# Performance work log

Hardware: AMD Instinct MI355X
Metric: run time of the kernel (lower is better)

Reference implementation:

```python
import jax, jax.numpy as jnp
import numpy as np

N = 100000
E = 3200000
NFEAT, NHID, NCLASS = 512, 64, 64
K = 10
ALPHA = 0.1


def setup_inputs() -> dict:
    key = jax.random.key(0)
    ks = jax.random.split(key, 8)
    x = jax.random.normal(ks[0], (N, NFEAT), dtype=jnp.float32)
    edge_index = jax.random.randint(ks[1], (2, E), 0, N, dtype=jnp.int32)
    s1 = 1.0 / np.sqrt(NFEAT)
    W1 = jax.random.uniform(ks[2], (NFEAT, NHID), jnp.float32, -s1, s1)
    b1 = jax.random.uniform(ks[3], (NHID,), jnp.float32, -s1, s1)
    s2 = 1.0 / np.sqrt(NHID)
    W2 = jax.random.uniform(ks[4], (NHID, NCLASS), jnp.float32, -s2, s2)
    b2 = jax.random.uniform(ks[5], (NCLASS,), jnp.float32, -s2, s2)
    # PPR init of gamma coefficients: temp[k] = alpha*(1-alpha)^k, temp[K] = (1-alpha)^K
    temp = ALPHA * (1.0 - ALPHA) ** np.arange(K + 1)
    temp[-1] = (1.0 - ALPHA) ** K
    temp = jnp.asarray(temp, dtype=jnp.float32)
    return {"x": x, "edge_index": edge_index, "W1": W1, "b1": b1, "W2": W2, "b2": b2, "temp": temp}


def _gcn_norm(edge_index, num_nodes):
    # add self loops, weight 1 (PyG gcn_norm defaults)
    loop = jnp.arange(num_nodes, dtype=edge_index.dtype)
    src = jnp.concatenate([edge_index[0], loop])
    dst = jnp.concatenate([edge_index[1], loop])
    w = jnp.ones(src.shape[0], dtype=jnp.float32)
    deg = jax.ops.segment_sum(w, dst, num_segments=num_nodes)
    dinv = jnp.where(deg > 0, jax.lax.rsqrt(deg), 0.0)
    norm = dinv[src] * w * dinv[dst]
    return src, dst, norm


def reference(x, edge_index, W1, b1, W2, b2, temp):
    # MLP part (eval mode, dropout is identity)
    h = jax.nn.relu(x @ W1 + b1) @ W2 + b2  # [N, nclass]
    src, dst, norm = _gcn_norm(edge_index, x.shape[0])
    hidden = h * temp[0]
    for k in range(K):
        # gather-scale-scatter: h <- A_hat @ h
        h = jax.ops.segment_sum(norm[:, None] * h[src], dst, num_segments=x.shape[0])
        hidden = hidden + temp[k + 1] * h
    return hidden
```

## Files before the change

### kernel.cpp

```cpp
#include <hip/hip_runtime.h>

static constexpr int N = 100000;
static constexpr int E = 3200000;
static constexpr int NFEAT = 512;
static constexpr int K = 10;

typedef _Float16 half8 __attribute__((ext_vector_type(8)));
typedef _Float16 half4v __attribute__((ext_vector_type(4)));
typedef float v2f __attribute__((ext_vector_type(2)));
typedef unsigned int uint2v __attribute__((ext_vector_type(2)));

static constexpr size_t OFF_CNT    = 0;
static constexpr size_t OFF_FILL   = 512ull * 1024;
static constexpr size_t OFF_ROWPTR = 1024ull * 1024;
static constexpr size_t OFF_DINV   = 1536ull * 1024;
static constexpr size_t OFF_BSUM   = 2048ull * 1024;
static constexpr size_t OFF_EW     = 2560ull * 1024;
static constexpr size_t OFF_G16    = OFF_EW + (size_t)E * 4 + 1024;
static constexpr size_t OFF_GA     = OFF_G16 + (size_t)N * 64 * 2 + 1024;
static constexpr size_t OFF_GB     = OFF_GA + (size_t)N * 64 + 1024;
static constexpr size_t OFF_SCA    = OFF_GB + (size_t)N * 64 + 1024;
static constexpr size_t OFF_SCB    = OFF_SCA + (size_t)N * 4 + 1024;
static constexpr size_t OFF_H1     = OFF_SCB + (size_t)N * 4 + 1024;

__global__ __launch_bounds__(256) void count_k(const int* __restrict__ dst,
                                               int* __restrict__ cnt) {
  int e = blockIdx.x * 256 + threadIdx.x;
  if (e < E) atomicAdd(&cnt[__builtin_nontemporal_load(dst + e)], 1);
}

__global__ __launch_bounds__(256) void dinv_k(const int* __restrict__ cnt,
                                              float* __restrict__ dinv) {
  int i = blockIdx.x * 256 + threadIdx.x;
  if (i < N) dinv[i] = 1.0f / sqrtf((float)(cnt[i] + 1));
}

__device__ inline int wave_incl_scan(int x) {
  int lane = threadIdx.x & 63;
#pragma unroll
  for (int off = 1; off < 64; off <<= 1) {
    int y = __shfl_up(x, off, 64);
    if (lane >= off) x += y;
  }
  return x;
}

__global__ __launch_bounds__(256) void scan1_k(const int* __restrict__ cnt,
                                               int* __restrict__ rowptr,
                                               int* __restrict__ bsum) {
  __shared__ int wsum[4];
  int tid = threadIdx.x, wid = tid >> 6, lane = tid & 63;
  int base = blockIdx.x * 1024 + tid * 4;
  int4 v = {0, 0, 0, 0};
  if (base + 3 < N) {
    v = *(const int4*)(cnt + base);
  } else {
    if (base + 0 < N) v.x = cnt[base + 0];
    if (base + 1 < N) v.y = cnt[base + 1];
    if (base + 2 < N) v.z = cnt[base + 2];
    if (base + 3 < N) v.w = cnt[base + 3];
  }
  int tsum = v.x + v.y + v.z + v.w;
  int incl = wave_incl_scan(tsum);
  if (lane == 63) wsum[wid] = incl;
  __syncthreads();
  int wof = 0;
  for (int i = 0; i < wid; ++i) wof += wsum[i];
  int e0 = wof + incl - tsum;
  if (base + 0 < N) rowptr[base + 0] = e0;
  if (base + 1 < N) rowptr[base + 1] = e0 + v.x;
  if (base + 2 < N) rowptr[base + 2] = e0 + v.x + v.y;
  if (base + 3 < N) rowptr[base + 3] = e0 + v.x + v.y + v.z;
  if (tid == 255) bsum[blockIdx.x] = wof + incl;
}

__global__ __launch_bounds__(128) void scan2_k(int* __restrict__ bsum) {
  __shared__ int w0sum;
  int tid = threadIdx.x, wid = tid >> 6, lane = tid & 63;
  int v = (tid < 98) ? bsum[tid] : 0;
  int incl = wave_incl_scan(v);
  if (wid == 0 && lane == 63) w0sum = incl;
  __syncthreads();
  int excl = incl - v + (wid ? w0sum : 0);
  if (tid < 98) bsum[tid] = excl;
}

__global__ __launch_bounds__(256) void scan3_k(int* __restrict__ rowptr,
                                               const int* __restrict__ bsum) {
  int i = blockIdx.x * 256 + threadIdx.x;
  if (i < N) rowptr[i] += bsum[blockIdx.x >> 2];
  if (i == 0) rowptr[N] = E;
}

__global__ __launch_bounds__(256) void fill2_k(const int* __restrict__ src,
                                               const int* __restrict__ dst,
                                               const int* __restrict__ rowptr,
                                               int* __restrict__ fillc,
                                               int* __restrict__ es) {
  const int slice = blockIdx.x & 7;
  const int chunk = blockIdx.x >> 3;
  const int lo = slice * 12500;
  const int hi = lo + 12500;
  int e = chunk * 4096 + threadIdx.x;
  const int eend = min(E, chunk * 4096 + 4096);
  for (; e < eend; e += 256) {
    int d = __builtin_nontemporal_load(dst + e);
    if (d >= lo && d < hi) {
      int pos = rowptr[d] + atomicAdd(&fillc[d], 1);
      es[pos] = __builtin_nontemporal_load(src + e);
    }
  }
}

__global__ __launch_bounds__(256) void gemm1_k(const float* __restrict__ x,
                                               const float* __restrict__ W1,
                                               const float* __restrict__ b1,
                                               _Float16* __restrict__ h1) {
  __shared__ float xs[16][256];
  __shared__ float w1s[16 * 64];
  const int tid = threadIdx.x;
  const int n0 = blockIdx.x * 256;
  const int tn = tid & 127;
  const int jh = tid >> 7;
  float4 acca[8], accb[8];
#pragma unroll
  for (int i = 0; i < 8; ++i) {
    acca[i] = float4{0.f, 0.f, 0.f, 0.f};
    accb[i] = float4{0.f, 0.f, 0.f, 0.f};
  }
  const int rowA = min(n0 + tid, N - 1);
  const float* xr = x + (size_t)rowA * NFEAT;
  for (int k0 = 0; k0 < NFEAT; k0 += 16) {
    float4 a0 = *(const float4*)(xr + k0 + 0);
    float4 a1 = *(const float4*)(xr + k0 + 4);
    float4 a2 = *(const float4*)(xr + k0 + 8);
    float4 a3 = *(const float4*)(xr + k0 + 12);
    float4 wv = *(const float4*)(W1 + (size_t)k0 * 64 + tid * 4);
    __syncthreads();
    xs[0][tid] = a0.x;  xs[1][tid] = a0.y;  xs[2][tid] = a0.z;  xs[3][tid] = a0.w;
    xs[4][tid] = a1.x;  xs[5][tid] = a1.y;  xs[6][tid] = a1.z;  xs[7][tid] = a1.w;
    xs[8][tid] = a2.x;  xs[9][tid] = a2.y;  xs[10][tid] = a2.z; xs[11][tid] = a2.w;
    xs[12][tid] = a3.x; xs[13][tid] = a3.y; xs[14][tid] = a3.z; xs[15][tid] = a3.w;
    *(float4*)&w1s[tid * 4] = wv;
    __syncthreads();
#pragma unroll
    for (int kk = 0; kk < 16; ++kk) {
      float xa = xs[kk][tn];
      float xb = xs[kk][tn + 128];
      const float* wr = &w1s[kk * 64 + jh * 32];
#pragma unroll
      for (int jj = 0; jj < 8; ++jj) {
        float4 w4 = *(const float4*)(wr + jj * 4);
        acca[jj].x += xa * w4.x; acca[jj].y += xa * w4.y;
        acca[jj].z += xa * w4.z; acca[jj].w += xa * w4.w;
        accb[jj].x += xb * w4.x; accb[jj].y += xb * w4.y;
        accb[jj].z += xb * w4.z; accb[jj].w += xb * w4.w;
      }
    }
  }
  const int na = n0 + tn, nb = na + 128;
#pragma unroll
  for (int jj = 0; jj < 8; ++jj) {
    int j = jh * 32 + jj * 4;
    float4 bb = *(const float4*)(b1 + j);
    half4v ra, rb;
    ra[0] = (_Float16)fmaxf(acca[jj].x + bb.x, 0.f);
    ra[1] = (_Float16)fmaxf(acca[jj].y + bb.y, 0.f);
    ra[2] = (_Float16)fmaxf(acca[jj].z + bb.z, 0.f);
    ra[3] = (_Float16)fmaxf(acca[jj].w + bb.w, 0.f);
    rb[0] = (_Float16)fmaxf(accb[jj].x + bb.x, 0.f);
    rb[1] = (_Float16)fmaxf(accb[jj].y + bb.y, 0.f);
    rb[2] = (_Float16)fmaxf(accb[jj].z + bb.z, 0.f);
    rb[3] = (_Float16)fmaxf(accb[jj].w + bb.w, 0.f);
    if (na < N) *(half4v*)(h1 + (size_t)na * 64 + j) = ra;
    if (nb < N) *(half4v*)(h1 + (size_t)nb * 64 + j) = rb;
  }
}

__global__ __launch_bounds__(256) void gemm2_k(const _Float16* __restrict__ h1,
                                               const float* __restrict__ W2,
                                               const float* __restrict__ b2,
                                               const float* __restrict__ temp,
                                               const float* __restrict__ dinv,
                                               _Float16* __restrict__ g16,
                                               float* __restrict__ out) {
  __shared__ float w2s[64 * 64];
  const int tid = threadIdx.x;
#pragma unroll
  for (int i = 0; i < 4; ++i)
    *(float4*)&w2s[(i * 256 + tid) * 4] = *(const float4*)(W2 + (size_t)(i * 256 + tid) * 4);
  __syncthreads();
  const int node = blockIdx.x * 256 + tid;
  if (node >= N) return;
  float4 acc[16];
#pragma unroll
  for (int c = 0; c < 16; ++c) acc[c] = *(const float4*)(b2 + c * 4);
  const _Float16* hr = h1 + (size_t)node * 64;
  for (int j0 = 0; j0 < 64; j0 += 8) {
    half8 hv = *(const half8*)(hr + j0);
#pragma unroll
    for (int l = 0; l < 8; ++l) {
      float hl = (float)hv[l];
      const float* wr = &w2s[(j0 + l) * 64];
#pragma unroll
      for (int c = 0; c < 16; ++c) {
        float4 w4 = *(const float4*)(wr + c * 4);
        acc[c].x += hl * w4.x; acc[c].y += hl * w4.y;
        acc[c].z += hl * w4.z; acc[c].w += hl * w4.w;
      }
    }
  }
  const float t0 = temp[0];
  const float di = dinv[node];
  float* op = out + (size_t)node * 64;
  _Float16* gp = g16 + (size_t)node * 64;
#pragma unroll
  for (int c = 0; c < 16; ++c) {
    const float4 a = acc[c];
    float4 o;
    o.x = t0 * a.x; o.y = t0 * a.y; o.z = t0 * a.z; o.w = t0 * a.w;
    *(float4*)(op + c * 4) = o;
    half4v g;
    g[0] = (_Float16)(di * a.x); g[1] = (_Float16)(di * a.y);
    g[2] = (_Float16)(di * a.z); g[3] = (_Float16)(di * a.w);
    *(half4v*)(gp + c * 4) = g;
  }
}

__device__ inline void dec8(uint2v u, float* f) {
  v2f p0 = __builtin_amdgcn_cvt_pk_f32_fp8(u.x, false);
  v2f p1 = __builtin_amdgcn_cvt_pk_f32_fp8(u.x, true);
  v2f p2 = __builtin_amdgcn_cvt_pk_f32_fp8(u.y, false);
  v2f p3 = __builtin_amdgcn_cvt_pk_f32_fp8(u.y, true);
  f[0] = p0.x; f[1] = p0.y; f[2] = p1.x; f[3] = p1.y;
  f[4] = p2.x; f[5] = p2.y; f[6] = p3.x; f[7] = p3.y;
}

__device__ inline void write_fp8_state(const float* S, float dd, int node, int l,
                                       unsigned int* __restrict__ gout,
                                       float* __restrict__ oscale) {
  float v[8];
#pragma unroll
  for (int i = 0; i < 8; ++i) v[i] = dd * S[i];
  float m = 0.f;
#pragma unroll
  for (int i = 0; i < 8; ++i) m = fmaxf(m, fabsf(v[i]));
#pragma unroll
  for (int off = 1; off < 8; off <<= 1) m = fmaxf(m, __shfl_xor(m, off, 64));
  const float esc = (m > 0.f) ? 240.0f / m : 0.f;
  if (l == 0) oscale[node] = m * (1.0f / 240.0f);
  unsigned int w0 = 0, w1 = 0;
  w0 = __builtin_amdgcn_cvt_pk_fp8_f32(v[0] * esc, v[1] * esc, w0, false);
  w0 = __builtin_amdgcn_cvt_pk_fp8_f32(v[2] * esc, v[3] * esc, w0, true);
  w1 = __builtin_amdgcn_cvt_pk_fp8_f32(v[4] * esc, v[5] * esc, w1, false);
  w1 = __builtin_amdgcn_cvt_pk_fp8_f32(v[6] * esc, v[7] * esc, w1, true);
  uint2v gw; gw.x = w0; gw.y = w1;
  *(uint2v*)(gout + (size_t)node * 16 + l * 2) = gw;
}

__global__ __launch_bounds__(256) void prop16_k(const _Float16* __restrict__ gin,
                                                unsigned int* __restrict__ gout,
                                                float* __restrict__ oscale,
                                                float* __restrict__ out,
                                                const int* __restrict__ rowptr,
                                                const int* __restrict__ es,
                                                const float* __restrict__ dinv,
                                                const float* __restrict__ temp) {
  const int tid = threadIdx.x;
  const int sub = tid >> 3;
  const int l = tid & 7;
  const int node = blockIdx.x * 32 + sub;
  const int rs = rowptr[node];
  const int re = rowptr[node + 1];
  const float di = dinv[node];
  const _Float16* __restrict__ gq = gin + l * 8;

  half8 sr = *(const half8*)(gq + (size_t)node * 64);
  float a0[8], a1[8], a2[8], a3[8];
#pragma unroll
  for (int i = 0; i < 8; ++i) {
    a0[i] = (float)sr[i];
    a1[i] = 0.f; a2[i] = 0.f; a3[i] = 0.f;
  }

  int e = rs;
  for (; e + 4 <= re; e += 4) {
    int s0 = es[e], s1 = es[e + 1], s2 = es[e + 2], s3 = es[e + 3];
    half8 r0 = *(const half8*)(gq + (size_t)s0 * 64);
    half8 r1 = *(const half8*)(gq + (size_t)s1 * 64);
    half8 r2 = *(const half8*)(gq + (size_t)s2 * 64);
    half8 r3 = *(const half8*)(gq + (size_t)s3 * 64);
#pragma unroll
    for (int i = 0; i < 8; ++i) {
      a0[i] += (float)r0[i];
      a1[i] += (float)r1[i];
      a2[i] += (float)r2[i];
      a3[i] += (float)r3[i];
    }
  }
  for (; e < re; ++e) {
    int s0 = es[e];
    half8 r0 = *(const half8*)(gq + (size_t)s0 * 64);
#pragma unroll
    for (int i = 0; i < 8; ++i) a0[i] += (float)r0[i];
  }

  float S[8];
#pragma unroll
  for (int i = 0; i < 8; ++i) S[i] = (a0[i] + a1[i]) + (a2[i] + a3[i]);

  const float th = temp[1] * di;
  const float dd = di * di;
  const size_t base = (size_t)node * 64 + l * 8;
  float4 o0 = *(const float4*)(out + base);
  float4 o1 = *(const float4*)(out + base + 4);
  o0.x += th * S[0]; o0.y += th * S[1]; o0.z += th * S[2]; o0.w += th * S[3];
  o1.x += th * S[4]; o1.y += th * S[5]; o1.z += th * S[6]; o1.w += th * S[7];
  *(float4*)(out + base) = o0;
  *(float4*)(out + base + 4) = o1;
  write_fp8_state(S, dd, node, l, gout, oscale);
}

__global__ __launch_bounds__(256) void prop8_k(const unsigned int* __restrict__ gin,
                                               const float* __restrict__ iscale,
                                               unsigned int* __restrict__ gout,
                                               float* __restrict__ oscale,
                                               float* __restrict__ out,
                                               const int* __restrict__ rowptr,
                                               const int* __restrict__ es,
                                               const float* __restrict__ dinv,
                                               const float* __restrict__ temp,
                                               int kp1, int writeh) {
  const int tid = threadIdx.x;
  const int sub = tid >> 3;
  const int l = tid & 7;
  const int node = blockIdx.x * 32 + sub;
  const int rs = rowptr[node];
  const int re = rowptr[node + 1];
  const float di = dinv[node];
  const unsigned int* __restrict__ gq = gin + l * 2;

  uint2v sv = *(const uint2v*)(gq + (size_t)node * 16);
  const float sci = iscale[node];
  float t8[8];
  dec8(sv, t8);
  float a0[8], a1[8], a2[8], a3[8];
#pragma unroll
  for (int i = 0; i < 8; ++i) {
    a0[i] = sci * t8[i];
    a1[i] = 0.f; a2[i] = 0.f; a3[i] = 0.f;
  }

  int e = rs;
  for (; e + 4 <= re; e += 4) {
    int s0 = es[e], s1 = es[e + 1], s2 = es[e + 2], s3 = es[e + 3];
    float sc0 = iscale[s0], sc1 = iscale[s1], sc2 = iscale[s2], sc3 = iscale[s3];
    uint2v u0 = *(const uint2v*)(gq + (size_t)s0 * 16);
    uint2v u1 = *(const uint2v*)(gq + (size_t)s1 * 16);
    uint2v u2 = *(const uint2v*)(gq + (size_t)s2 * 16);
    uint2v u3 = *(const uint2v*)(gq + (size_t)s3 * 16);
    float r0[8], r1[8], r2[8], r3[8];
    dec8(u0, r0); dec8(u1, r1); dec8(u2, r2); dec8(u3, r3);
#pragma unroll
    for (int i = 0; i < 8; ++i) {
      a0[i] += sc0 * r0[i];
      a1[i] += sc1 * r1[i];
      a2[i] += sc2 * r2[i];
      a3[i] += sc3 * r3[i];
    }
  }
  for (; e < re; ++e) {
    int s0 = es[e];
    float sc0 = iscale[s0];
    uint2v u0 = *(const uint2v*)(gq + (size_t)s0 * 16);
    float r0[8];
    dec8(u0, r0);
#pragma unroll
    for (int i = 0; i < 8; ++i) a0[i] += sc0 * r0[i];
  }

  float S[8];
#pragma unroll
  for (int i = 0; i < 8; ++i) S[i] = (a0[i] + a1[i]) + (a2[i] + a3[i]);

  const float th = temp[kp1] * di;
  const float dd = di * di;
  const size_t base = (size_t)node * 64 + l * 8;
  float4 o0 = *(const float4*)(out + base);
  float4 o1 = *(const float4*)(out + base + 4);
  o0.x += th * S[0]; o0.y += th * S[1]; o0.z += th * S[2]; o0.w += th * S[3];
  o1.x += th * S[4]; o1.y += th * S[5]; o1.z += th * S[6]; o1.w += th * S[7];
  *(float4*)(out + base) = o0;
  *(float4*)(out + base + 4) = o1;
  if (writeh) write_fp8_state(S, dd, node, l, gout, oscale);
}

extern "C" void kernel_launch(void* const* d_in, const int* in_sizes, int n_in,
                              void* d_out, int out_size, void* d_ws, size_t ws_size,
                              hipStream_t stream) {
  const float* x = (const float*)d_in[0];
  const int* ei = (const int*)d_in[1];
  const float* W1 = (const float*)d_in[2];
  const float* b1 = (const float*)d_in[3];
  const float* W2 = (const float*)d_in[4];
  const float* b2 = (const float*)d_in[5];
  const float* temp = (const float*)d_in[6];
  const int* srcp = ei;
  const int* dstp = ei + E;

  unsigned char* ws = (unsigned char*)d_ws;
  int* cnt = (int*)(ws + OFF_CNT);
  int* fillc = (int*)(ws + OFF_FILL);
  int* rowptr = (int*)(ws + OFF_ROWPTR);
  float* dinv = (float*)(ws + OFF_DINV);
  int* bsum = (int*)(ws + OFF_BSUM);
  int* es = (int*)(ws + OFF_EW);
  _Float16* g16 = (_Float16*)(ws + OFF_G16);
  unsigned int* gA = (unsigned int*)(ws + OFF_GA);
  unsigned int* gB = (unsigned int*)(ws + OFF_GB);
  float* scA = (float*)(ws + OFF_SCA);
  float* scB = (float*)(ws + OFF_SCB);
  _Float16* h1 = (_Float16*)(ws + OFF_H1);
  float* out = (float*)d_out;

  hipMemsetAsync(cnt, 0, (size_t)N * 4, stream);
  hipMemsetAsync(fillc, 0, (size_t)N * 4, stream);

  count_k<<<E / 256, 256, 0, stream>>>(dstp, cnt);
  dinv_k<<<(N + 255) / 256, 256, 0, stream>>>(cnt, dinv);
  scan1_k<<<(N + 1023) / 1024, 256, 0, stream>>>(cnt, rowptr, bsum);
  scan2_k<<<1, 128, 0, stream>>>(bsum);
  scan3_k<<<(N + 255) / 256, 256, 0, stream>>>(rowptr, bsum);
  fill2_k<<<8 * 782, 256, 0, stream>>>(srcp, dstp, rowptr, fillc, es);

  gemm1_k<<<(N + 255) / 256, 256, 0, stream>>>(x, W1, b1, h1);
  gemm2_k<<<(N + 255) / 256, 256, 0, stream>>>(h1, W2, b2, temp, dinv, g16, out);

  prop16_k<<<N / 32, 256, 0, stream>>>(g16, gA, scA, out, rowptr, es, dinv, temp);

  const unsigned int* gin = gA;
  unsigned int* gout = gB;
  const float* sin = scA;
  float* sout = scB;
  for (int k = 1; k < K; ++k) {
    prop8_k<<<N / 32, 256, 0, stream>>>(gin, sin, gout, sout, out, rowptr, es,
                                        dinv, temp, k + 1, (k + 1 < K) ? 1 : 0);
    const unsigned int* tg = gin; gin = gout; gout = (unsigned int*)tg;
    const float* ts = sin; sin = sout; sout = (float*)ts;
  }
}
```

Before: 1.026 ms.

## Make CSR fill persistent with XCC-affine destination slices via atomic chunk counters

The CSR fill kernel becomes persistent. Each block reads its XCC id and claims edge chunks through per-slice atomic counters, starting with the destination slice matching its XCC and then moving on to the other slices. The goal is to keep each destination range's fill-counter atomics and rowptr reads local to one XCC's L2, cutting cross-die traffic. In exchange it adds a global atomic and two barriers per chunk, and the write order within rows becomes nondeterministic.

Measured after the change: 1.213 ms. +18.1%, slower.

```diff
diff --git a/kernel.cpp b/kernel.cpp
--- a/kernel.cpp
+++ b/kernel.cpp
@@ -4,6 +4,7 @@
 static constexpr int E = 3200000;
 static constexpr int NFEAT = 512;
 static constexpr int K = 10;
+static constexpr int NCHUNK = (E + 4095) / 4096;
 
 typedef _Float16 half8 __attribute__((ext_vector_type(8)));
 typedef _Float16 half4v __attribute__((ext_vector_type(4)));
@@ -15,6 +16,7 @@
 static constexpr size_t OFF_ROWPTR = 1024ull * 1024;
 static constexpr size_t OFF_DINV   = 1536ull * 1024;
 static constexpr size_t OFF_BSUM   = 2048ull * 1024;
+static constexpr size_t OFF_CCTR   = 2304ull * 1024;
 static constexpr size_t OFF_EW     = 2560ull * 1024;
 static constexpr size_t OFF_G16    = OFF_EW + (size_t)E * 4 + 1024;
 static constexpr size_t OFF_GA     = OFF_G16 + (size_t)N * 64 * 2 + 1024;
@@ -92,22 +94,34 @@
   if (i == 0) rowptr[N] = E;
 }
 
-__global__ __launch_bounds__(256) void fill2_k(const int* __restrict__ src,
+__global__ __launch_bounds__(256) void fill3_k(const int* __restrict__ src,
                                                const int* __restrict__ dst,
                                                const int* __restrict__ rowptr,
                                                int* __restrict__ fillc,
+                                               int* __restrict__ cctr,
                                                int* __restrict__ es) {
-  const int slice = blockIdx.x & 7;
-  const int chunk = blockIdx.x >> 3;
-  const int lo = slice * 12500;
-  const int hi = lo + 12500;
-  int e = chunk * 4096 + threadIdx.x;
-  const int eend = min(E, chunk * 4096 + 4096);
-  for (; e < eend; e += 256) {
-    int d = __builtin_nontemporal_load(dst + e);
-    if (d >= lo && d < hi) {
-      int pos = rowptr[d] + atomicAdd(&fillc[d], 1);
-      es[pos] = __builtin_nontemporal_load(src + e);
+  int xcc;
+  asm("s_getreg_b32 %0, hwreg(HW_REG_XCC_ID)" : "=s"(xcc));
+  __shared__ int sc;
+  for (int soff = 0; soff < 8; ++soff) {
+    const int slice = (xcc + soff) & 7;
+    const int lo = slice * 12500;
+    const int hi = lo + 12500;
+    for (;;) {
+      __syncthreads();
+      if (threadIdx.x == 0) sc = atomicAdd(&cctr[slice], 1);
+      __syncthreads();
+      const int c = sc;
+      if (c >= NCHUNK) break;
+      const int e0 = c * 4096;
+      const int eend = min(E, e0 + 4096);
+      for (int e = e0 + threadIdx.x; e < eend; e += 256) {
+        int d = __builtin_nontemporal_load(dst + e);
+        if (d >= lo && d < hi) {
+          int pos = rowptr[d] + atomicAdd(&fillc[d], 1);
+          es[pos] = __builtin_nontemporal_load(src + e);
+        }
+      }
     }
   }
 }
@@ -414,6 +428,7 @@
   int* rowptr = (int*)(ws + OFF_ROWPTR);
   float* dinv = (float*)(ws + OFF_DINV);
   int* bsum = (int*)(ws + OFF_BSUM);
+  int* cctr = (int*)(ws + OFF_CCTR);
   int* es = (int*)(ws + OFF_EW);
   _Float16* g16 = (_Float16*)(ws + OFF_G16);
   unsigned int* gA = (unsigned int*)(ws + OFF_GA);
@@ -425,13 +440,14 @@
 
   hipMemsetAsync(cnt, 0, (size_t)N * 4, stream);
   hipMemsetAsync(fillc, 0, (size_t)N * 4, stream);
+  hipMemsetAsync(cctr, 0, 8 * 4, stream);
 
   count_k<<<E / 256, 256, 0, stream>>>(dstp, cnt);
   dinv_k<<<(N + 255) / 256, 256, 0, stream>>>(cnt, dinv);
   scan1_k<<<(N + 1023) / 1024, 256, 0, stream>>>(cnt, rowptr, bsum);
   scan2_k<<<1, 128, 0, stream>>>(bsum);
   scan3_k<<<(N + 255) / 256, 256, 0, stream>>>(rowptr, bsum);
-  fill2_k<<<8 * 782, 256, 0, stream>>>(srcp, dstp, rowptr, fillc, es);
+  fill3_k<<<2048, 256, 0, stream>>>(srcp, dstp, rowptr, fillc, cctr, es);
 
   gemm1_k<<<(N + 255) / 256, 256, 0, stream>>>(x, W1, b1, h1);
   gemm2_k<<<(N + 255) / 256, 256, 0, stream>>>(h1, W2, b2, temp, dinv, g16, out);
```

## Split propagation into two passes by source-node half for gather locality

Applied to the files above, without the earlier changes.

Each node's CSR edge list is partitioned by whether the source index falls in the lower or upper half of the nodes, using extra counters and a mid pointer. Each propagation step then runs two kernels: the first gathers only low-half sources and writes an fp32 partial sum, the second gathers high-half sources and adds the partial. The aim is to shrink each pass's gather working set so it fits better in cache. In exchange it adds a kernel launch per step, a 25.6MB partial write and read per step, and extra preprocessing atomics and memsets.

Measured after the change: 1.192 ms. +16.1%, slower.

```diff
diff --git a/kernel.cpp b/kernel.cpp
--- a/kernel.cpp
+++ b/kernel.cpp
@@ -4,29 +4,41 @@
 static constexpr int E = 3200000;
 static constexpr int NFEAT = 512;
 static constexpr int K = 10;
+static constexpr int HALF = 50000;
 
 typedef _Float16 half8 __attribute__((ext_vector_type(8)));
 typedef _Float16 half4v __attribute__((ext_vector_type(4)));
 typedef float v2f __attribute__((ext_vector_type(2)));
+typedef float float4nt __attribute__((ext_vector_type(4)));
 typedef unsigned int uint2v __attribute__((ext_vector_type(2)));
 
 static constexpr size_t OFF_CNT    = 0;
-static constexpr size_t OFF_FILL   = 512ull * 1024;
-static constexpr size_t OFF_ROWPTR = 1024ull * 1024;
-static constexpr size_t OFF_DINV   = 1536ull * 1024;
-static constexpr size_t OFF_BSUM   = 2048ull * 1024;
-static constexpr size_t OFF_EW     = 2560ull * 1024;
-static constexpr size_t OFF_G16    = OFF_EW + (size_t)E * 4 + 1024;
-static constexpr size_t OFF_GA     = OFF_G16 + (size_t)N * 64 * 2 + 1024;
+static constexpr size_t OFF_CNTA   = 512ull * 1024;
+static constexpr size_t OFF_FILLA  = 1024ull * 1024;
+static constexpr size_t OFF_FILLB  = 1536ull * 1024;
+static constexpr size_t OFF_ROWPTR = 2048ull * 1024;
+static constexpr size_t OFF_MID    = 2560ull * 1024;
+static constexpr size_t OFF_DINV   = 3072ull * 1024;
+static constexpr size_t OFF_BSUM   = 3584ull * 1024;
+static constexpr size_t OFF_EW     = 4096ull * 1024;
+static constexpr size_t OFF_GA     = OFF_EW + (size_t)E * 4 + 1024;
 static constexpr size_t OFF_GB     = OFF_GA + (size_t)N * 64 + 1024;
 static constexpr size_t OFF_SCA    = OFF_GB + (size_t)N * 64 + 1024;
 static constexpr size_t OFF_SCB    = OFF_SCA + (size_t)N * 4 + 1024;
-static constexpr size_t OFF_H1     = OFF_SCB + (size_t)N * 4 + 1024;
-
-__global__ __launch_bounds__(256) void count_k(const int* __restrict__ dst,
-                                               int* __restrict__ cnt) {
+static constexpr size_t OFF_G16    = OFF_SCB + (size_t)N * 4 + 1024;
+static constexpr size_t OFF_H1     = OFF_G16 + (size_t)N * 128 + 1024;
+static constexpr size_t OFF_PART   = OFF_G16;
+
+__global__ __launch_bounds__(256) void count_k(const int* __restrict__ src,
+                                               const int* __restrict__ dst,
+                                               int* __restrict__ cnt,
+                                               int* __restrict__ cntA) {
   int e = blockIdx.x * 256 + threadIdx.x;
-  if (e < E) atomicAdd(&cnt[__builtin_nontemporal_load(dst + e)], 1);
+  if (e >= E) return;
+  int d = __builtin_nontemporal_load(dst + e);
+  int s = __builtin_nontemporal_load(src + e);
+  atomicAdd(&cnt[d], 1);
+  if (s < HALF) atomicAdd(&cntA[d], 1);
 }
 
 __global__ __launch_bounds__(256) void dinv_k(const int* __restrict__ cnt,
@@ -92,10 +104,19 @@
   if (i == 0) rowptr[N] = E;
 }
 
+__global__ __launch_bounds__(256) void mid_k(const int* __restrict__ rowptr,
+                                             const int* __restrict__ cntA,
+                                             int* __restrict__ mid) {
+  int i = blockIdx.x * 256 + threadIdx.x;
+  if (i < N) mid[i] = rowptr[i] + cntA[i];
+}
+
 __global__ __launch_bounds__(256) void fill2_k(const int* __restrict__ src,
                                                const int* __restrict__ dst,
                                                const int* __restrict__ rowptr,
-                                               int* __restrict__ fillc,
+                                               const int* __restrict__ mid,
+                                               int* __restrict__ fillA,
+                                               int* __restrict__ fillB,
                                                int* __restrict__ es) {
   const int slice = blockIdx.x & 7;
   const int chunk = blockIdx.x >> 3;
@@ -106,8 +127,10 @@
   for (; e < eend; e += 256) {
     int d = __builtin_nontemporal_load(dst + e);
     if (d >= lo && d < hi) {
-      int pos = rowptr[d] + atomicAdd(&fillc[d], 1);
-      es[pos] = __builtin_nontemporal_load(src + e);
+      int s = __builtin_nontemporal_load(src + e);
+      int pos = (s < HALF) ? rowptr[d] + atomicAdd(&fillA[d], 1)
+                           : mid[d] + atomicAdd(&fillB[d], 1);
+      es[pos] = s;
     }
   }
 }
@@ -321,35 +344,23 @@
   write_fp8_state(S, dd, node, l, gout, oscale);
 }
 
-__global__ __launch_bounds__(256) void prop8_k(const unsigned int* __restrict__ gin,
-                                               const float* __restrict__ iscale,
-                                               unsigned int* __restrict__ gout,
-                                               float* __restrict__ oscale,
-                                               float* __restrict__ out,
-                                               const int* __restrict__ rowptr,
-                                               const int* __restrict__ es,
-                                               const float* __restrict__ dinv,
-                                               const float* __restrict__ temp,
-                                               int kp1, int writeh) {
+__global__ __launch_bounds__(256) void propA8_k(const unsigned int* __restrict__ gin,
+                                                const float* __restrict__ iscale,
+                                                float* __restrict__ partial,
+                                                const int* __restrict__ rowptr,
+                                                const int* __restrict__ mid,
+                                                const int* __restrict__ es) {
   const int tid = threadIdx.x;
   const int sub = tid >> 3;
   const int l = tid & 7;
   const int node = blockIdx.x * 32 + sub;
   const int rs = rowptr[node];
-  const int re = rowptr[node + 1];
-  const float di = dinv[node];
+  const int re = mid[node];
   const unsigned int* __restrict__ gq = gin + l * 2;
 
-  uint2v sv = *(const uint2v*)(gq + (size_t)node * 16);
-  const float sci = iscale[node];
-  float t8[8];
-  dec8(sv, t8);
   float a0[8], a1[8], a2[8], a3[8];
 #pragma unroll
-  for (int i = 0; i < 8; ++i) {
-    a0[i] = sci * t8[i];
-    a1[i] = 0.f; a2[i] = 0.f; a3[i] = 0.f;
-  }
+  for (int i = 0; i < 8; ++i) { a0[i] = 0.f; a1[i] = 0.f; a2[i] = 0.f; a3[i] = 0.f; }
 
   int e = rs;
   for (; e + 4 <= re; e += 4) {
@@ -379,13 +390,95 @@
     for (int i = 0; i < 8; ++i) a0[i] += sc0 * r0[i];
   }
 
+  const size_t base = (size_t)node * 64 + l * 8;
+  float4nt p0, p1;
+  p0.x = (a0[0] + a1[0]) + (a2[0] + a3[0]);
+  p0.y = (a0[1] + a1[1]) + (a2[1] + a3[1]);
+  p0.z = (a0[2] + a1[2]) + (a2[2] + a3[2]);
+  p0.w = (a0[3] + a1[3]) + (a2[3] + a3[3]);
+  p1.x = (a0[4] + a1[4]) + (a2[4] + a3[4]);
+  p1.y = (a0[5] + a1[5]) + (a2[5] + a3[5]);
+  p1.z = (a0[6] + a1[6]) + (a2[6] + a3[6]);
+  p1.w = (a0[7] + a1[7]) + (a2[7] + a3[7]);
+  __builtin_nontemporal_store(p0, (float4nt*)(partial + base));
+  __builtin_nontemporal_store(p1, (float4nt*)(partial + base + 4));
+}
+
+__global__ __launch_bounds__(256) void propB8_k(const unsigned int* __restrict__ gin,
+                                                const float* __restrict__ iscale,
+                                                const float* __restrict__ partial,
+                                                unsigned int* __restrict__ gout,
+                                                float* __restrict__ oscale,
+                                                float* __restrict__ out,
+                                                const int* __restrict__ rowptr,
+                                                const int* __restrict__ mid,
+                                                const int* __restrict__ es,
+                                                const float* __restrict__ dinv,
+                                                const float* __restrict__ temp,
+                                                int kp1, int writeh) {
+  const int tid = threadIdx.x;
+  const int sub = tid >> 3;
+  const int l = tid & 7;
+  const int node = blockIdx.x * 32 + sub;
+  const int rs = mid[node];
+  const int re = rowptr[node + 1];
+  const float di = dinv[node];
+  const unsigned int* __restrict__ gq = gin + l * 2;
+
+  uint2v sv = *(const uint2v*)(gq + (size_t)node * 16);
+  const float sci = iscale[node];
+  float t8[8];
+  dec8(sv, t8);
+  float a0[8], a1[8], a2[8], a3[8];
+#pragma unroll
+  for (int i = 0; i < 8; ++i) {
+    a0[i] = sci * t8[i];
+    a1[i] = 0.f; a2[i] = 0.f; a3[i] = 0.f;
+  }
+
+  int e = rs;
+  for (; e + 4 <= re; e += 4) {
+    int s0 = es[e], s1 = es[e + 1], s2 = es[e + 2], s3 = es[e + 3];
+    float sc0 = iscale[s0], sc1 = iscale[s1], sc2 = iscale[s2], sc3 = iscale[s3];
+    uint2v u0 = *(const uint2v*)(gq + (size_t)s0 * 16);
+    uint2v u1 = *(const uint2v*)(gq + (size_t)s1 * 16);
+    uint2v u2 = *(const uint2v*)(gq + (size_t)s2 * 16);
+    uint2v u3 = *(const uint2v*)(gq + (size_t)s3 * 16);
+    float r0[8], r1[8], r2[8], r3[8];
+    dec8(u0, r0); dec8(u1, r1); dec8(u2, r2); dec8(u3, r3);
+#pragma unroll
+    for (int i = 0; i < 8; ++i) {
+      a0[i] += sc0 * r0[i];
+      a1[i] += sc1 * r1[i];
+      a2[i] += sc2 * r2[i];
+      a3[i] += sc3 * r3[i];
+    }
+  }
+  for (; e < re; ++e) {
+    int s0 = es[e];
+    float sc0 = iscale[s0];
+    uint2v u0 = *(const uint2v*)(gq + (size_t)s0 * 16);
+    float r0[8];
+    dec8(u0, r0);
+#pragma unroll
+    for (int i = 0; i < 8; ++i) a0[i] += sc0 * r0[i];
+  }
+
+  const size_t base = (size_t)node * 64 + l * 8;
+  float4nt pp0 = __builtin_nontemporal_load((const float4nt*)(partial + base));
+  float4nt pp1 = __builtin_nontemporal_load((const float4nt*)(partial + base + 4));
   float S[8];
-#pragma unroll
-  for (int i = 0; i < 8; ++i) S[i] = (a0[i] + a1[i]) + (a2[i] + a3[i]);
+  S[0] = (a0[0] + a1[0]) + (a2[0] + a3[0]) + pp0.x;
+  S[1] = (a0[1] + a1[1]) + (a2[1] + a3[1]) + pp0.y;
+  S[2] = (a0[2] + a1[2]) + (a2[2] + a3[2]) + pp0.z;
+  S[3] = (a0[3] + a1[3]) + (a2[3] + a3[3]) + pp0.w;
+  S[4] = (a0[4] + a1[4]) + (a2[4] + a3[4]) + pp1.x;
+  S[5] = (a0[5] + a1[5]) + (a2[5] + a3[5]) + pp1.y;
+  S[6] = (a0[6] + a1[6]) + (a2[6] + a3[6]) + pp1.z;
+  S[7] = (a0[7] + a1[7]) + (a2[7] + a3[7]) + pp1.w;
 
   const float th = temp[kp1] * di;
   const float dd = di * di;
-  const size_t base = (size_t)node * 64 + l * 8;
   float4 o0 = *(const float4*)(out + base);
   float4 o1 = *(const float4*)(out + base + 4);
   o0.x += th * S[0]; o0.y += th * S[1]; o0.z += th * S[2]; o0.w += th * S[3];
@@ -410,28 +503,35 @@
 
   unsigned char* ws = (unsigned char*)d_ws;
   int* cnt = (int*)(ws + OFF_CNT);
-  int* fillc = (int*)(ws + OFF_FILL);
+  int* cntA = (int*)(ws + OFF_CNTA);
+  int* fillA = (int*)(ws + OFF_FILLA);
+  int* fillB = (int*)(ws + OFF_FILLB);
   int* rowptr = (int*)(ws + OFF_ROWPTR);
+  int* mid = (int*)(ws + OFF_MID);
   float* dinv = (float*)(ws + OFF_DINV);
   int* bsum = (int*)(ws + OFF_BSUM);
   int* es = (int*)(ws + OFF_EW);
-  _Float16* g16 = (_Float16*)(ws + OFF_G16);
   unsigned int* gA = (unsigned int*)(ws + OFF_GA);
   unsigned int* gB = (unsigned int*)(ws + OFF_GB);
   float* scA = (float*)(ws + OFF_SCA);
   float* scB = (float*)(ws + OFF_SCB);
+  _Float16* g16 = (_Float16*)(ws + OFF_G16);
   _Float16* h1 = (_Float16*)(ws + OFF_H1);
+  float* partial = (float*)(ws + OFF_PART);
   float* out = (float*)d_out;
 
   hipMemsetAsync(cnt, 0, (size_t)N * 4, stream);
-  hipMemsetAsync(fillc, 0, (size_t)N * 4, stream);
-
-  count_k<<<E / 256, 256, 0, stream>>>(dstp, cnt);
+  hipMemsetAsync(cntA, 0, (size_t)N * 4, stream);
+  hipMemsetAsync(fillA, 0, (size_t)N * 4, stream);
+  hipMemsetAsync(fillB, 0, (size_t)N * 4, stream);
+
+  count_k<<<E / 256, 256, 0, stream>>>(srcp, dstp, cnt, cntA);
   dinv_k<<<(N + 255) / 256, 256, 0, stream>>>(cnt, dinv);
   scan1_k<<<(N + 1023) / 1024, 256, 0, stream>>>(cnt, rowptr, bsum);
   scan2_k<<<1, 128, 0, stream>>>(bsum);
   scan3_k<<<(N + 255) / 256, 256, 0, stream>>>(rowptr, bsum);
-  fill2_k<<<8 * 782, 256, 0, stream>>>(srcp, dstp, rowptr, fillc, es);
+  mid_k<<<(N + 255) / 256, 256, 0, stream>>>(rowptr, cntA, mid);
+  fill2_k<<<8 * 782, 256, 0, stream>>>(srcp, dstp, rowptr, mid, fillA, fillB, es);
 
   gemm1_k<<<(N + 255) / 256, 256, 0, stream>>>(x, W1, b1, h1);
   gemm2_k<<<(N + 255) / 256, 256, 0, stream>>>(h1, W2, b2, temp, dinv, g16, out);
@@ -443,8 +543,10 @@
   const float* sin = scA;
   float* sout = scB;
   for (int k = 1; k < K; ++k) {
-    prop8_k<<<N / 32, 256, 0, stream>>>(gin, sin, gout, sout, out, rowptr, es,
-                                        dinv, temp, k + 1, (k + 1 < K) ? 1 : 0);
+    propA8_k<<<N / 32, 256, 0, stream>>>(gin, sin, partial, rowptr, mid, es);
+    propB8_k<<<N / 32, 256, 0, stream>>>(gin, sin, partial, gout, sout, out,
+                                         rowptr, mid, es, dinv, temp, k + 1,
+                                         (k + 1 < K) ? 1 : 0);
     const unsigned int* tg = gin; gin = gout; gout = (unsigned int*)tg;
     const float* ts = sin; sin = sout; sout = (float*)ts;
   }
```

## Map one wavefront per node in fp8 propagation with byte-per-lane gathers

Applied to the files above, without the earlier changes.

The fp8 propagation kernel now assigns a full 64-lane wavefront to each node, with each lane handling one feature byte, instead of 8 lanes per node each loading 8 bytes. Edge bounds are made wave-uniform via readfirstlane, the edge loop is unrolled by 8 with independent accumulators, and the per-node max reduction spans the whole wave. This is meant to cut divergence from varying degrees across nodes in a wave and to raise memory-level parallelism. The cost is narrower byte loads per lane, more per-edge index and scale loads across lanes, and eight times as many blocks.

Result: slower. 1.329 ms (+29.5%).

```diff
diff --git a/kernel.cpp b/kernel.cpp
--- a/kernel.cpp
+++ b/kernel.cpp
@@ -17,11 +17,16 @@
 static constexpr size_t OFF_BSUM   = 2048ull * 1024;
 static constexpr size_t OFF_EW     = 2560ull * 1024;
 static constexpr size_t OFF_G16    = OFF_EW + (size_t)E * 4 + 1024;
-static constexpr size_t OFF_GA     = OFF_G16 + (size_t)N * 64 * 2 + 1024;
+static constexpr size_t OFF_GA     = OFF_G16 + (size_t)N * 128 + 1024;
 static constexpr size_t OFF_GB     = OFF_GA + (size_t)N * 64 + 1024;
 static constexpr size_t OFF_SCA    = OFF_GB + (size_t)N * 64 + 1024;
 static constexpr size_t OFF_SCB    = OFF_SCA + (size_t)N * 4 + 1024;
 static constexpr size_t OFF_H1     = OFF_SCB + (size_t)N * 4 + 1024;
+
+__device__ inline float dec1(int b) {
+  v2f p = __builtin_amdgcn_cvt_pk_f32_fp8(b, false);
+  return p[0];
+}
 
 __global__ __launch_bounds__(256) void count_k(const int* __restrict__ dst,
                                                int* __restrict__ cnt) {
@@ -227,15 +232,6 @@
   }
 }
 
-__device__ inline void dec8(uint2v u, float* f) {
-  v2f p0 = __builtin_amdgcn_cvt_pk_f32_fp8(u.x, false);
-  v2f p1 = __builtin_amdgcn_cvt_pk_f32_fp8(u.x, true);
-  v2f p2 = __builtin_amdgcn_cvt_pk_f32_fp8(u.y, false);
-  v2f p3 = __builtin_amdgcn_cvt_pk_f32_fp8(u.y, true);
-  f[0] = p0.x; f[1] = p0.y; f[2] = p1.x; f[3] = p1.y;
-  f[4] = p2.x; f[5] = p2.y; f[6] = p3.x; f[7] = p3.y;
-}
-
 __device__ inline void write_fp8_state(const float* S, float dd, int node, int l,
                                        unsigned int* __restrict__ gout,
                                        float* __restrict__ oscale) {
@@ -321,9 +317,9 @@
   write_fp8_state(S, dd, node, l, gout, oscale);
 }
 
-__global__ __launch_bounds__(256) void prop8_k(const unsigned int* __restrict__ gin,
+__global__ __launch_bounds__(256) void prop8_k(const unsigned char* __restrict__ gin,
                                                const float* __restrict__ iscale,
-                                               unsigned int* __restrict__ gout,
+                                               unsigned char* __restrict__ gout,
                                                float* __restrict__ oscale,
                                                float* __restrict__ out,
                                                const int* __restrict__ rowptr,
@@ -331,68 +327,61 @@
                                                const float* __restrict__ dinv,
                                                const float* __restrict__ temp,
                                                int kp1, int writeh) {
-  const int tid = threadIdx.x;
-  const int sub = tid >> 3;
-  const int l = tid & 7;
-  const int node = blockIdx.x * 32 + sub;
-  const int rs = rowptr[node];
-  const int re = rowptr[node + 1];
+  const int lane = threadIdx.x & 63;
+  const int node = blockIdx.x * 4 + (threadIdx.x >> 6);
+  const int rs = __builtin_amdgcn_readfirstlane(rowptr[node]);
+  const int re = __builtin_amdgcn_readfirstlane(rowptr[node + 1]);
   const float di = dinv[node];
-  const unsigned int* __restrict__ gq = gin + l * 2;
-
-  uint2v sv = *(const uint2v*)(gq + (size_t)node * 16);
-  const float sci = iscale[node];
-  float t8[8];
-  dec8(sv, t8);
-  float a0[8], a1[8], a2[8], a3[8];
-#pragma unroll
-  for (int i = 0; i < 8; ++i) {
-    a0[i] = sci * t8[i];
-    a1[i] = 0.f; a2[i] = 0.f; a3[i] = 0.f;
-  }
+
+  float a0 = iscale[node] * dec1((int)gin[(size_t)node * 64 + lane]);
+  float a1 = 0.f, a2 = 0.f, a3 = 0.f;
+  float a4 = 0.f, a5 = 0.f, a6 = 0.f, a7 = 0.f;
 
   int e = rs;
-  for (; e + 4 <= re; e += 4) {
-    int s0 = es[e], s1 = es[e + 1], s2 = es[e + 2], s3 = es[e + 3];
-    float sc0 = iscale[s0], sc1 = iscale[s1], sc2 = iscale[s2], sc3 = iscale[s3];
-    uint2v u0 = *(const uint2v*)(gq + (size_t)s0 * 16);
-    uint2v u1 = *(const uint2v*)(gq + (size_t)s1 * 16);
-    uint2v u2 = *(const uint2v*)(gq + (size_t)s2 * 16);
-    uint2v u3 = *(const uint2v*)(gq + (size_t)s3 * 16);
-    float r0[8], r1[8], r2[8], r3[8];
-    dec8(u0, r0); dec8(u1, r1); dec8(u2, r2); dec8(u3, r3);
-#pragma unroll
-    for (int i = 0; i < 8; ++i) {
-      a0[i] += sc0 * r0[i];
-      a1[i] += sc1 * r1[i];
-      a2[i] += sc2 * r2[i];
-      a3[i] += sc3 * r3[i];
-    }
+  for (; e + 8 <= re; e += 8) {
+    int s0 = es[e],     s1 = es[e + 1], s2 = es[e + 2], s3 = es[e + 3];
+    int s4 = es[e + 4], s5 = es[e + 5], s6 = es[e + 6], s7 = es[e + 7];
+    float c0 = iscale[s0], c1 = iscale[s1], c2 = iscale[s2], c3 = iscale[s3];
+    float c4 = iscale[s4], c5 = iscale[s5], c6 = iscale[s6], c7 = iscale[s7];
+    int b0 = gin[(size_t)s0 * 64 + lane];
+    int b1 = gin[(size_t)s1 * 64 + lane];
+    int b2 = gin[(size_t)s2 * 64 + lane];
+    int b3 = gin[(size_t)s3 * 64 + lane];
+    int b4 = gin[(size_t)s4 * 64 + lane];
+    int b5 = gin[(size_t)s5 * 64 + lane];
+    int b6 = gin[(size_t)s6 * 64 + lane];
+    int b7 = gin[(size_t)s7 * 64 + lane];
+    a0 += c0 * dec1(b0);
+    a1 += c1 * dec1(b1);
+    a2 += c2 * dec1(b2);
+    a3 += c3 * dec1(b3);
+    a4 += c4 * dec1(b4);
+    a5 += c5 * dec1(b5);
+    a6 += c6 * dec1(b6);
+    a7 += c7 * dec1(b7);
   }
   for (; e < re; ++e) {
     int s0 = es[e];
-    float sc0 = iscale[s0];
-    uint2v u0 = *(const uint2v*)(gq + (size_t)s0 * 16);
-    float r0[8];
-    dec8(u0, r0);
-#pragma unroll
-    for (int i = 0; i < 8; ++i) a0[i] += sc0 * r0[i];
-  }
-
-  float S[8];
-#pragma unroll
-  for (int i = 0; i < 8; ++i) S[i] = (a0[i] + a1[i]) + (a2[i] + a3[i]);
+    float c0 = iscale[s0];
+    int b0 = gin[(size_t)s0 * 64 + lane];
+    a0 += c0 * dec1(b0);
+  }
+
+  const float S = ((a0 + a1) + (a2 + a3)) + ((a4 + a5) + (a6 + a7));
 
   const float th = temp[kp1] * di;
-  const float dd = di * di;
-  const size_t base = (size_t)node * 64 + l * 8;
-  float4 o0 = *(const float4*)(out + base);
-  float4 o1 = *(const float4*)(out + base + 4);
-  o0.x += th * S[0]; o0.y += th * S[1]; o0.z += th * S[2]; o0.w += th * S[3];
-  o1.x += th * S[4]; o1.y += th * S[5]; o1.z += th * S[6]; o1.w += th * S[7];
-  *(float4*)(out + base) = o0;
-  *(float4*)(out + base + 4) = o1;
-  if (writeh) write_fp8_state(S, dd, node, l, gout, oscale);
+  const size_t base = (size_t)node * 64 + lane;
+  out[base] += th * S;
+  if (writeh) {
+    const float v = di * di * S;
+    float m = fabsf(v);
+#pragma unroll
+    for (int off = 1; off < 64; off <<= 1) m = fmaxf(m, __shfl_xor(m, off, 64));
+    const float esc = (m > 0.f) ? 240.0f / m : 0.f;
+    if (lane == 0) oscale[node] = m * (1.0f / 240.0f);
+    unsigned int w = __builtin_amdgcn_cvt_pk_fp8_f32(v * esc, v * esc, 0u, false);
+    gout[base] = (unsigned char)(w & 0xFF);
+  }
 }
 
 extern "C" void kernel_launch(void* const* d_in, const int* in_sizes, int n_in,
@@ -416,8 +405,8 @@
   int* bsum = (int*)(ws + OFF_BSUM);
   int* es = (int*)(ws + OFF_EW);
   _Float16* g16 = (_Float16*)(ws + OFF_G16);
-  unsigned int* gA = (unsigned int*)(ws + OFF_GA);
-  unsigned int* gB = (unsigned int*)(ws + OFF_GB);
+  unsigned char* gA = (unsigned char*)(ws + OFF_GA);
+  unsigned char* gB = (unsigned char*)(ws + OFF_GB);
   float* scA = (float*)(ws + OFF_SCA);
   float* scB = (float*)(ws + OFF_SCB);
   _Float16* h1 = (_Float16*)(ws + OFF_H1);
@@ -436,16 +425,17 @@
   gemm1_k<<<(N + 255) / 256, 256, 0, stream>>>(x, W1, b1, h1);
   gemm2_k<<<(N + 255) / 256, 256, 0, stream>>>(h1, W2, b2, temp, dinv, g16, out);
 
-  prop16_k<<<N / 32, 256, 0, stream>>>(g16, gA, scA, out, rowptr, es, dinv, temp);
-
-  const unsigned int* gin = gA;
-  unsigned int* gout = gB;
+  prop16_k<<<N / 32, 256, 0, stream>>>(g16, (unsigned int*)gA, scA, out, rowptr,
+                                       es, dinv, temp);
+
+  const unsigned char* gin = gA;
+  unsigned char* gout = gB;
   const float* sin = scA;
   float* sout = scB;
   for (int k = 1; k < K; ++k) {
-    prop8_k<<<N / 32, 256, 0, stream>>>(gin, sin, gout, sout, out, rowptr, es,
-                                        dinv, temp, k + 1, (k + 1 < K) ? 1 : 0);
-    const unsigned int* tg = gin; gin = gout; gout = (unsigned int*)tg;
+    prop8_k<<<N / 4, 256, 0, stream>>>(gin, sin, gout, sout, out, rowptr, es,
+                                       dinv, temp, k + 1, (k + 1 < K) ? 1 : 0);
+    const unsigned char* tg = gin; gin = gout; gout = (unsigned char*)tg;
     const float* ts = sin; sin = sout; sout = (float*)ts;
   }
 }
```
